# Performance work log

Hardware: AMD Instinct MI355X
Metric: run time of the kernel (lower is better)

The kernel has to match this reference:

```python
import jax, jax.numpy as jnp
import numpy as np

N = 2_097_152   # number of samples
C = 16          # n_classes
DECAY = 0.8


def setup_inputs() -> dict:
    key = jax.random.key(0)
    k1, k2 = jax.random.split(key)
    logits = jax.random.normal(k1, (N, C), dtype=jnp.float32)
    targets = jax.random.randint(k2, (N,), 0, C)
    weight = jnp.ones((C,), dtype=jnp.float32)  # EMA class-weight buffer
    return {"logits": logits, "targets": targets, "weight": weight}


def reference(logits, targets, weight):
    # Single-pass histogram (replaces the per-class Python loop in the source)
    counts = jax.ops.segment_sum(
        jnp.ones_like(targets, dtype=logits.dtype), targets, num_segments=C
    )  # [C]
    new_w = counts.sum() / counts          # total / per-class count
    new_w = new_w / new_w.sum()            # normalize to sum 1
    w = DECAY * weight + (1.0 - DECAY) * new_w  # EMA-updated weight [C]

    # Weighted cross-entropy, mean reduction (torch semantics:
    # sum(w[y_i] * nll_i) / sum(w[y_i]))
    logp = jax.nn.log_softmax(logits, axis=-1)                       # [N, C]
    nll = -jnp.take_along_axis(logp, targets[:, None], axis=-1)[:, 0]  # [N]
    sw = w[targets]                                                  # [N]
    return jnp.sum(sw * nll) / jnp.sum(sw)
```

## Files before the change

### kernel.cpp

```cpp
#include <hip/hip_runtime.h>

#define NCLS 16
#define DECAY 0.8f

__device__ __forceinline__ float sel16(float4 q0, float4 q1, float4 q2,
                                       float4 q3, int t) {
    float4 sv = (t & 8) ? ((t & 4) ? q3 : q2) : ((t & 4) ? q1 : q0);
    const float lo = (t & 1) ? sv.y : sv.x;
    const float hi = (t & 1) ? sv.w : sv.z;
    return (t & 2) ? hi : lo;
}

__device__ __forceinline__ float esum4(float4 v) {
    return __expf(v.x) + __expf(v.y) + __expf(v.z) + __expf(v.w);
}

__global__ void __launch_bounds__(256, 8)
dwce_fused_kernel(const float4* __restrict__ logits4,
                  const int*    __restrict__ targets,
                  float2* __restrict__ partials, int n) {
    __shared__ unsigned int cnt[4][NCLS];
    __shared__ float       snll[4][NCLS];

    const int tid = threadIdx.x;
    const int wid = tid >> 6;
    if (tid < 64) { cnt[tid >> 4][tid & 15] = 0u; snll[tid >> 4][tid & 15] = 0.f; }
    __syncthreads();

    const int gid  = blockIdx.x * blockDim.x + tid;
    const int nth  = gridDim.x * blockDim.x;
    const int half = n >> 1;

    for (int i = gid; i < half; i += nth) {
        const float4* ra = logits4 + (size_t)i * 4;
        const float4* rb = logits4 + ((size_t)i + half) * 4;
        float4 a0 = ra[0], a1 = ra[1], a2 = ra[2], a3 = ra[3];
        float4 b0 = rb[0], b1 = rb[1], b2 = rb[2], b3 = rb[3];
        const int ta = targets[i];
        const int tb = targets[i + half];

        const float Sa = esum4(a0) + esum4(a1) + esum4(a2) + esum4(a3);
        const float Sb = esum4(b0) + esum4(b1) + esum4(b2) + esum4(b3);
        const float xa = sel16(a0, a1, a2, a3, ta);
        const float xb = sel16(b0, b1, b2, b3, tb);

        atomicAdd(&snll[wid][ta], __logf(Sa) - xa);
        atomicAdd(&snll[wid][tb], __logf(Sb) - xb);
        atomicAdd(&cnt[wid][ta], 1u);
        atomicAdd(&cnt[wid][tb], 1u);
    }
    __syncthreads();

    if (tid < NCLS) {
        const unsigned int c =
            cnt[0][tid] + cnt[1][tid] + cnt[2][tid] + cnt[3][tid];
        const float s =
            snll[0][tid] + snll[1][tid] + snll[2][tid] + snll[3][tid];
        partials[tid * gridDim.x + blockIdx.x] = make_float2((float)c, s);
    }
}

__global__ void __launch_bounds__(1024)
dwce_final_kernel(const float2* __restrict__ partials,
                  const float*  __restrict__ weight,
                  int nb, int n, float* __restrict__ out) {
    const int tid  = threadIdx.x;
    const int c    = tid >> 6;
    const int lane = tid & 63;

    float  cacc = 0.f;
    double sacc = 0.0;
    for (int b = lane; b < nb; b += 64) {
        const float2 p = partials[c * nb + b];
        cacc += p.x;
        sacc += (double)p.y;
    }
    #pragma unroll
    for (int off = 32; off > 0; off >>= 1) {
        cacc += __shfl_xor(cacc, off);
        sacc += __shfl_xor(sacc, off);
    }

    __shared__ float  scnt[NCLS];
    __shared__ double ssum[NCLS];
    if (lane == 0) { scnt[c] = cacc; ssum[c] = sacc; }
    __syncthreads();

    if (tid < NCLS) {
        const float  cn = scnt[tid];
        const double sn = ssum[tid];

        const float raw = (float)n / cn;
        float s = raw;
        s += __shfl_xor(s, 1);
        s += __shfl_xor(s, 2);
        s += __shfl_xor(s, 4);
        s += __shfl_xor(s, 8);
        const float w = DECAY * weight[tid] + (1.0f - DECAY) * (raw / s);

        double A = (double)w * sn;
        double B = (double)w * (double)cn;
        A += __shfl_xor(A, 1); B += __shfl_xor(B, 1);
        A += __shfl_xor(A, 2); B += __shfl_xor(B, 2);
        A += __shfl_xor(A, 4); B += __shfl_xor(B, 4);
        A += __shfl_xor(A, 8); B += __shfl_xor(B, 8);
        if (tid == 0) out[0] = (float)(A / B);
    }
}

extern "C" void kernel_launch(void* const* d_in, const int* in_sizes, int n_in,
                              void* d_out, int out_size, void* d_ws, size_t ws_size,
                              hipStream_t stream) {
    const float* logits  = (const float*)d_in[0];
    const int*   targets = (const int*)d_in[1];
    const float* weight  = (const float*)d_in[2];
    float* out = (float*)d_out;

    float2* partials = (float2*)d_ws;

    const int n = in_sizes[1];

    int nb = 4096;
    const int ws_cap = (int)(ws_size / (NCLS * sizeof(float2)));
    if (nb > ws_cap) nb = ws_cap;
    if (nb < 1) nb = 1;

    dwce_fused_kernel<<<nb, 256, 0, stream>>>((const float4*)logits, targets,
                                              partials, n);
    dwce_final_kernel<<<1, 1024, 0, stream>>>(partials, weight, nb, n, out);
}
```

Baseline: 45.89 us.

## Split each row across lane pairs and combine halves with DPP swaps

```diff
diff --git a/kernel.cpp b/kernel.cpp
--- a/kernel.cpp
+++ b/kernel.cpp
@@ -3,19 +3,24 @@
 #define NCLS 16
 #define DECAY 0.8f
 
-__device__ __forceinline__ float sel16(float4 q0, float4 q1, float4 q2,
-                                       float4 q3, int t) {
-    float4 sv = (t & 8) ? ((t & 4) ? q3 : q2) : ((t & 4) ? q1 : q0);
+__device__ __forceinline__ float esum4(float4 v) {
+    return __expf(v.x) + __expf(v.y) + __expf(v.z) + __expf(v.w);
+}
+
+__device__ __forceinline__ float dpp_xor1(float x) {
+    int i = __builtin_bit_cast(int, x);
+    i = __builtin_amdgcn_mov_dpp(i, 0xB1, 0xF, 0xF, true);
+    return __builtin_bit_cast(float, i);
+}
+
+__device__ __forceinline__ float sel8(float4 q0, float4 q1, int t) {
+    float4 sv = (t & 4) ? q1 : q0;
     const float lo = (t & 1) ? sv.y : sv.x;
     const float hi = (t & 1) ? sv.w : sv.z;
     return (t & 2) ? hi : lo;
 }
 
-__device__ __forceinline__ float esum4(float4 v) {
-    return __expf(v.x) + __expf(v.y) + __expf(v.z) + __expf(v.w);
-}
-
-__global__ void __launch_bounds__(256, 8)
+__global__ void __launch_bounds__(256)
 dwce_fused_kernel(const float4* __restrict__ logits4,
                   const int*    __restrict__ targets,
                   float2* __restrict__ partials, int n) {
@@ -27,27 +32,47 @@
     if (tid < 64) { cnt[tid >> 4][tid & 15] = 0u; snll[tid >> 4][tid & 15] = 0.f; }
     __syncthreads();
 
-    const int gid  = blockIdx.x * blockDim.x + tid;
-    const int nth  = gridDim.x * blockDim.x;
-    const int half = n >> 1;
+    const int gid = blockIdx.x * blockDim.x + tid;
+    const int nth = gridDim.x * blockDim.x;
+    const int nh  = n << 1;
 
-    for (int i = gid; i < half; i += nth) {
-        const float4* ra = logits4 + (size_t)i * 4;
-        const float4* rb = logits4 + ((size_t)i + half) * 4;
-        float4 a0 = ra[0], a1 = ra[1], a2 = ra[2], a3 = ra[3];
-        float4 b0 = rb[0], b1 = rb[1], b2 = rb[2], b3 = rb[3];
-        const int ta = targets[i];
-        const int tb = targets[i + half];
+    for (int h0 = gid; h0 < nh; h0 += 2 * nth) {
+        const int h1 = h0 + nth;
+        const bool do1 = (h1 < nh);
 
-        const float Sa = esum4(a0) + esum4(a1) + esum4(a2) + esum4(a3);
-        const float Sb = esum4(b0) + esum4(b1) + esum4(b2) + esum4(b3);
-        const float xa = sel16(a0, a1, a2, a3, ta);
-        const float xb = sel16(b0, b1, b2, b3, tb);
+        const float4* p0 = logits4 + ((size_t)h0 << 1);
+        const float4 a0 = p0[0], a1 = p0[1];
+        const int r0 = h0 >> 1, s0 = h0 & 1;
+        const int t0 = targets[r0];
 
-        atomicAdd(&snll[wid][ta], __logf(Sa) - xa);
-        atomicAdd(&snll[wid][tb], __logf(Sb) - xb);
-        atomicAdd(&cnt[wid][ta], 1u);
-        atomicAdd(&cnt[wid][tb], 1u);
+        float4 b0, b1; int r1 = 0, s1 = 0, t1 = 0;
+        if (do1) {
+            const float4* p1 = logits4 + ((size_t)h1 << 1);
+            b0 = p1[0]; b1 = p1[1];
+            r1 = h1 >> 1; s1 = h1 & 1;
+            t1 = targets[r1];
+        }
+
+        {
+            const float e  = esum4(a0) + esum4(a1);
+            const float E  = e + dpp_xor1(e);
+            const float xl = ((t0 >> 3) == s0) ? sel8(a0, a1, t0 & 7) : 0.f;
+            const float X  = xl + dpp_xor1(xl);
+            if (s0 == 0) {
+                atomicAdd(&snll[wid][t0], __logf(E) - X);
+                atomicAdd(&cnt[wid][t0], 1u);
+            }
+        }
+        if (do1) {
+            const float e  = esum4(b0) + esum4(b1);
+            const float E  = e + dpp_xor1(e);
+            const float xl = ((t1 >> 3) == s1) ? sel8(b0, b1, t1 & 7) : 0.f;
+            const float X  = xl + dpp_xor1(xl);
+            if (s1 == 0) {
+                atomicAdd(&snll[wid][t1], __logf(E) - X);
+                atomicAdd(&cnt[wid][t1], 1u);
+            }
+        }
     }
     __syncthreads();
 
@@ -120,7 +145,7 @@
 
     const int n = in_sizes[1];
 
-    int nb = 4096;
+    int nb = 2048;
     const int ws_cap = (int)(ws_size / (NCLS * sizeof(float2)));
     if (nb > ws_cap) nb = ws_cap;
     if (nb < 1) nb = 1;
```

After: 38.19 us. 16.8% less time.
